# Performance work log

Measured on AMD Instinct MI355X. Metric: run time of the kernel, lower is better.

Reference implementation:

```python
import jax, jax.numpy as jnp
import numpy as np

N_EMBD = 1024
N_HEAD = 16

def _lin_params(key, fan_in, fan_out):
    kw, kb = jax.random.split(key)
    bound = 1.0 / np.sqrt(fan_in)
    W = jax.random.uniform(kw, (fan_in, fan_out), minval=-bound, maxval=bound, dtype=jnp.float32)
    b = jax.random.uniform(kb, (fan_out,), minval=-bound, maxval=bound, dtype=jnp.float32)
    return W, b

def setup_inputs() -> dict:
    key = jax.random.key(0)
    ks = jax.random.split(key, 6)
    x = jax.random.normal(ks[0], (2, 2048, N_EMBD), dtype=jnp.float32)
    W_attn, b_attn = _lin_params(ks[1], N_EMBD, 3 * N_EMBD)
    W_proj, b_proj = _lin_params(ks[2], N_EMBD, N_EMBD)
    W_fc, b_fc = _lin_params(ks[3], N_EMBD, 4 * N_EMBD)
    W_fc2, b_fc2 = _lin_params(ks[4], 4 * N_EMBD, N_EMBD)
    ln1_g = jnp.ones((N_EMBD,), jnp.float32); ln1_b = jnp.zeros((N_EMBD,), jnp.float32)
    ln2_g = jnp.ones((N_EMBD,), jnp.float32); ln2_b = jnp.zeros((N_EMBD,), jnp.float32)
    return {"x": x, "W_attn": W_attn, "b_attn": b_attn, "W_proj": W_proj, "b_proj": b_proj,
            "W_fc": W_fc, "b_fc": b_fc, "W_fc2": W_fc2, "b_fc2": b_fc2,
            "ln1_g": ln1_g, "ln1_b": ln1_b, "ln2_g": ln2_g, "ln2_b": ln2_b}

def _layernorm(x, g, b, eps=1e-5):
    mu = jnp.mean(x, axis=-1, keepdims=True)
    var = jnp.var(x, axis=-1, keepdims=True)
    return (x - mu) * jax.lax.rsqrt(var + eps) * g + b

def _attention(x, W_attn, b_attn, W_proj, b_proj):
    B, T, C = x.shape
    hd = C // N_HEAD
    qkv = x @ W_attn + b_attn                      # [B,T,3C]
    q, k, v = jnp.split(qkv, 3, axis=-1)
    # [B,T,C] -> [B,H,T,hd]
    q = q.reshape(B, T, N_HEAD, hd).transpose(0, 2, 1, 3)
    k = k.reshape(B, T, N_HEAD, hd).transpose(0, 2, 1, 3)
    v = v.reshape(B, T, N_HEAD, hd).transpose(0, 2, 1, 3)
    att = jnp.einsum('bhqd,bhkd->bhqk', q, k) * (1.0 / np.sqrt(hd))
    causal = jnp.tril(jnp.ones((T, T), bool))
    att = jnp.where(causal[None, None], att, -jnp.inf)
    att = jax.nn.softmax(att, axis=-1)
    y = jnp.einsum('bhqk,bhkd->bhqd', att, v)      # [B,H,T,hd]
    y = y.transpose(0, 2, 1, 3).reshape(B, T, C)
    return y @ W_proj + b_proj

def _mlp(x, W_fc, b_fc, W_fc2, b_fc2):
    h = jax.nn.gelu(x @ W_fc + b_fc, approximate=False)
    return h @ W_fc2 + b_fc2

def reference(x, W_attn, b_attn, W_proj, b_proj, W_fc, b_fc, W_fc2, b_fc2,
              ln1_g, ln1_b, ln2_g, ln2_b):
    x = x + _attention(_layernorm(x, ln1_g, ln1_b), W_attn, b_attn, W_proj, b_proj)
    x = x + _mlp(_layernorm(x, ln2_g, ln2_b), W_fc, b_fc, W_fc2, b_fc2)
    return x
```

## Files before the change

kernel.cpp:

```cpp
#include <hip/hip_runtime.h>
#include <cstdint>
#include <cstddef>


typedef unsigned short u16;
typedef short bf16x8 __attribute__((ext_vector_type(8)));
typedef float f32x4 __attribute__((ext_vector_type(4)));

#define C_EMBD 1024
#define T_SEQ  2048
#define N_BATCH 2
#define N_HEADS 16
#define HEAD_D 64
#define M_TOK  4096
#define Q_SCALE 0.18033688011112042f

__device__ __forceinline__ u16 f2b(float f) {
  union { float f; unsigned u; } v; v.f = f;
  unsigned r = (v.u + 0x7fffu + ((v.u >> 16) & 1u)) >> 16;
  return (u16)r;
}
__device__ __forceinline__ float b2f(u16 u) {
  union { unsigned u; float f; } v; v.u = ((unsigned)u) << 16;
  return v.f;
}
__device__ __forceinline__ unsigned pk2(float a, float b) {
  union { float f; unsigned u; } x, y; x.f = a; y.f = b;
  return __builtin_amdgcn_perm(y.u, x.u, 0x07060302u);
}
__device__ __forceinline__ void load_lds16(const void* g, void* l) {
  __builtin_amdgcn_global_load_lds(
      (const __attribute__((address_space(1))) void*)g,
      (__attribute__((address_space(3))) void*)l, 16, 0, 0);
}
__device__ __forceinline__ float gelu_fast(float x) {
  const float p = x * __builtin_fmaf(0.044715f * x, x, 1.0f);
  const float t = __builtin_amdgcn_exp2f(2.3021859215f * p);
  return x * t * __builtin_amdgcn_rcpf(t + 1.0f);
}

__global__ __launch_bounds__(256) void transpose_cast_all(
    const float* __restrict__ W0, u16* __restrict__ D0,
    const float* __restrict__ W1, u16* __restrict__ D1,
    const float* __restrict__ W2, u16* __restrict__ D2,
    const float* __restrict__ W3, u16* __restrict__ D3) {
  int id = blockIdx.x;
  const float* W; u16* D; int K, N, t;
  if (id < 3072)      { W = W0; D = D0; K = 1024; N = 3072; t = id; }
  else if (id < 4096) { W = W1; D = D1; K = 1024; N = 1024; t = id - 3072; }
  else if (id < 8192) { W = W2; D = D2; K = 1024; N = 4096; t = id - 4096; }
  else                { W = W3; D = D3; K = 4096; N = 1024; t = id - 8192; }
  const int nTN = N >> 5;
  const int n0 = (t % nTN) * 32, k0 = (t / nTN) * 32;
  __shared__ float tile[32][33];
  const int tx = threadIdx.x & 31, ty = threadIdx.x >> 5;
#pragma unroll
  for (int i = 0; i < 32; i += 8)
    tile[ty + i][tx] = W[(size_t)(k0 + ty + i) * N + n0 + tx];
  __syncthreads();
#pragma unroll
  for (int i = 0; i < 32; i += 8)
    D[(size_t)(n0 + ty + i) * K + k0 + tx] = f2b(tile[tx][ty + i]);
}

__global__ __launch_bounds__(256) void ln_cast(
    const float* __restrict__ X, const float* __restrict__ g,
    const float* __restrict__ b, u16* __restrict__ Y) {
  const int row = blockIdx.x;
  const int tid = threadIdx.x;
  const float4 v = ((const float4*)(X + (size_t)row * C_EMBD))[tid];
  float s = v.x + v.y + v.z + v.w;
  float ss = v.x * v.x + v.y * v.y + v.z * v.z + v.w * v.w;
#pragma unroll
  for (int off = 32; off > 0; off >>= 1) {
    s += __shfl_down(s, off, 64);
    ss += __shfl_down(ss, off, 64);
  }
  __shared__ float red[8];
  __shared__ float stats[2];
  const int wave = tid >> 6, lane = tid & 63;
  if (lane == 0) { red[wave] = s; red[4 + wave] = ss; }
  __syncthreads();
  if (tid == 0) {
    float S = red[0] + red[1] + red[2] + red[3];
    float SS = red[4] + red[5] + red[6] + red[7];
    float mu = S * (1.0f / C_EMBD);
    float var = SS * (1.0f / C_EMBD) - mu * mu;
    stats[0] = mu;
    stats[1] = rsqrtf(var + 1e-5f);
  }
  __syncthreads();
  const float mu = stats[0], rs = stats[1];
  const float4 gv = ((const float4*)g)[tid];
  const float4 bv = ((const float4*)b)[tid];
  ushort4 o;
  o.x = f2b((v.x - mu) * rs * gv.x + bv.x);
  o.y = f2b((v.y - mu) * rs * gv.y + bv.y);
  o.z = f2b((v.z - mu) * rs * gv.z + bv.z);
  o.w = f2b((v.w - mu) * rs * gv.w + bv.w);
  ((ushort4*)(Y + (size_t)row * C_EMBD))[tid] = o;
}

__global__ __launch_bounds__(256) void ln_reduce_cast(
    const float* __restrict__ P0, const float* __restrict__ P1,
    const float* __restrict__ bias, const float* __restrict__ res,
    const float* __restrict__ g, const float* __restrict__ b,
    float* __restrict__ X1, u16* __restrict__ Y) {
  const int row = blockIdx.x;
  const int tid = threadIdx.x;
  const size_t base = (size_t)row * C_EMBD;
  const float4 p0 = ((const float4*)(P0 + base))[tid];
  const float4 p1 = ((const float4*)(P1 + base))[tid];
  const float4 rr = ((const float4*)(res + base))[tid];
  const float4 bb = ((const float4*)bias)[tid];
  float4 v;
  v.x = p0.x + p1.x + rr.x + bb.x;
  v.y = p0.y + p1.y + rr.y + bb.y;
  v.z = p0.z + p1.z + rr.z + bb.z;
  v.w = p0.w + p1.w + rr.w + bb.w;
  ((float4*)(X1 + base))[tid] = v;
  float s = v.x + v.y + v.z + v.w;
  float ss = v.x * v.x + v.y * v.y + v.z * v.z + v.w * v.w;
#pragma unroll
  for (int off = 32; off > 0; off >>= 1) {
    s += __shfl_down(s, off, 64);
    ss += __shfl_down(ss, off, 64);
  }
  __shared__ float red[8];
  __shared__ float stats[2];
  const int wave = tid >> 6, lane = tid & 63;
  if (lane == 0) { red[wave] = s; red[4 + wave] = ss; }
  __syncthreads();
  if (tid == 0) {
    float S = red[0] + red[1] + red[2] + red[3];
    float SS = red[4] + red[5] + red[6] + red[7];
    float mu = S * (1.0f / C_EMBD);
    float var = SS * (1.0f / C_EMBD) - mu * mu;
    stats[0] = mu;
    stats[1] = rsqrtf(var + 1e-5f);
  }
  __syncthreads();
  const float mu = stats[0], rs = stats[1];
  const float4 gv = ((const float4*)g)[tid];
  const float4 bv = ((const float4*)b)[tid];
  ushort4 o;
  o.x = f2b((v.x - mu) * rs * gv.x + bv.x);
  o.y = f2b((v.y - mu) * rs * gv.y + bv.y);
  o.z = f2b((v.z - mu) * rs * gv.z + bv.z);
  o.w = f2b((v.w - mu) * rs * gv.w + bv.w);
  ((ushort4*)(Y + base))[tid] = o;
}

enum { EPI_BF16 = 0, EPI_GELU_BF16 = 2, EPI_PART = 3, EPI_QKV = 4 };

template <int EPI, int SPLIT>
__global__ __launch_bounds__(256) void gemm_bt(
    const u16* __restrict__ A, const u16* __restrict__ Bt,
    const float* __restrict__ bias,
    void* __restrict__ Cout, void* __restrict__ Cout2, void* __restrict__ Cout3,
    int M, int N, int K) {
  __shared__ u16 As[128 * 64];
  __shared__ u16 Bs[128 * 64];
  const int tid = threadIdx.x;
  const int wave = tid >> 6, lane = tid & 63;
  const int quad = lane >> 4, l16 = lane & 15;
  const int sw = l16 & 7;

  const int id = (int)blockIdx.y * (int)gridDim.x + (int)blockIdx.x;
  const int mt = ((id & 7) << 2) + ((id >> 3) & 3);
  const int nt_ = id >> 5;
  const int m0 = mt * 128, n0 = nt_ * 128;

  const int wm = (wave >> 1) * 64, wn = (wave & 1) * 64;

  f32x4 acc[4][4] = {};

  size_t aOff[4], bOff[4];
  int ldsOff[4];
#pragma unroll
  for (int i = 0; i < 4; ++i) {
    const int c = tid + i * 256;
    const int row = c >> 3, gc = ((c & 7) ^ (row & 7)) * 8;
    aOff[i] = (size_t)(m0 + row) * K + gc;
    bOff[i] = (size_t)(n0 + row) * K + gc;
    ldsOff[i] = c * 8;
  }

  const int kTiles = (K >> 6) / SPLIT;
  const int kt0 = (SPLIT == 2) ? (int)blockIdx.z * kTiles : 0;
  for (int kt = kt0; kt < kt0 + kTiles; ++kt) {
    const int k0 = kt << 6;
#pragma unroll
    for (int i = 0; i < 4; ++i)
      load_lds16(A + aOff[i] + k0, &As[ldsOff[i]]);
#pragma unroll
    for (int i = 0; i < 4; ++i)
      load_lds16(Bt + bOff[i] + k0, &Bs[ldsOff[i]]);
    __syncthreads();
#pragma unroll
    for (int ks = 0; ks < 2; ++ks) {
      bf16x8 aF[4], bF[4];
#pragma unroll
      for (int t = 0; t < 4; ++t) {
        aF[t] = *(const bf16x8*)
            &As[(wm + t * 16 + l16) * 64 + (((ks * 4 + quad) ^ sw) * 8)];
        bF[t] = *(const bf16x8*)
            &Bs[(wn + t * 16 + l16) * 64 + (((ks * 4 + quad) ^ sw) * 8)];
      }
#pragma unroll
      for (int tm = 0; tm < 4; ++tm)
#pragma unroll
        for (int tn = 0; tn < 4; ++tn)
          acc[tm][tn] = __builtin_amdgcn_mfma_f32_16x16x32_bf16(
              bF[tn], aF[tm], acc[tm][tn], 0, 0, 0);
    }
    __syncthreads();
  }

  float* Pz = (float*)((SPLIT == 2 && blockIdx.z == 1) ? Cout2 : Cout);
#pragma unroll
  for (int tm = 0; tm < 4; ++tm) {
    const int row = m0 + wm + tm * 16 + l16;
#pragma unroll
    for (int tn = 0; tn < 4; ++tn) {
      const int col = n0 + wn + tn * 16 + quad * 4;
      if constexpr (EPI == EPI_PART) {
        *(float4*)&Pz[(size_t)row * N + col] = *(float4*)&acc[tm][tn];
      } else {
        const float4 bz = *(const float4*)&bias[col];
        float v0 = acc[tm][tn][0] + bz.x, v1 = acc[tm][tn][1] + bz.y;
        float v2 = acc[tm][tn][2] + bz.z, v3 = acc[tm][tn][3] + bz.w;
        if constexpr (EPI == EPI_GELU_BF16) {
          v0 = gelu_fast(v0); v1 = gelu_fast(v1);
          v2 = gelu_fast(v2); v3 = gelu_fast(v3);
        }
        ushort4 o;
        o.x = f2b(v0); o.y = f2b(v1); o.z = f2b(v2); o.w = f2b(v3);
        *(ushort4*)&((u16*)Cout)[(size_t)row * N + col] = o;
      }
    }
  }
}

#define PHASE(MQ, NQ, STG, POST)                                              \
  {                                                                           \
    bf16x8 aF[4][2], bF[2][2];                                                \
    const u16* Ab_ = &lds[(size_t)((((MQ)*2 + par)) << 13)];                  \
    const u16* Bb_ = &lds[(size_t)(((2 + (NQ)) * 2 + par) << 13)];            \
    _Pragma("unroll") for (int t_ = 0; t_ < 4; ++t_)                          \
      _Pragma("unroll") for (int ks = 0; ks < 2; ++ks)                        \
        aF[t_][ks] = *(const bf16x8*)&Ab_[(wm * 64 + t_ * 16 + l16) * 64 +    \
                                          (((ks * 4 + quad) ^ sw) << 3)];     \
    _Pragma("unroll") for (int u_ = 0; u_ < 2; ++u_)                          \
      _Pragma("unroll") for (int ks = 0; ks < 2; ++ks)                        \
        bF[u_][ks] = *(const bf16x8*)&Bb_[(wn * 32 + u_ * 16 + l16) * 64 +    \
                                          (((ks * 4 + quad) ^ sw) << 3)];     \
    STG;                                                                      \
    __builtin_amdgcn_s_barrier();                                             \
    asm volatile("s_waitcnt lgkmcnt(0)" ::: "memory");                        \
    __builtin_amdgcn_s_setprio(1);                                            \
    _Pragma("unroll") for (int t_ = 0; t_ < 4; ++t_)                          \
      _Pragma("unroll") for (int u_ = 0; u_ < 2; ++u_)                        \
        _Pragma("unroll") for (int ks = 0; ks < 2; ++ks)                      \
          acc[(MQ)*4 + t_][(NQ)*2 + u_] =                                     \
              __builtin_amdgcn_mfma_f32_16x16x32_bf16(                        \
                  bF[u_][ks], aF[t_][ks], acc[(MQ)*4 + t_][(NQ)*2 + u_],      \
                  0, 0, 0);                                                   \
    __builtin_amdgcn_s_setprio(0);                                            \
    POST;                                                                     \
    __builtin_amdgcn_s_barrier();                                             \
  }

template <int EPI, int SPLIT>
__global__ __launch_bounds__(512, 2) void gemm256(
    const u16* __restrict__ A, const u16* __restrict__ Bt,
    const float* __restrict__ bias,
    void* __restrict__ Cout, void* __restrict__ Cout2,
    void* __restrict__ Cout3, void* __restrict__ Cout4,
    int M, int N, int K) {
  __shared__ u16 lds[8 * 8192];
  const int tid = threadIdx.x;
  const int lane = tid & 63;
  const int wave = tid >> 6;
  const int quad = lane >> 4, l16 = lane & 15;
  const int sw = l16 & 7;
  const int wm = wave >> 2, wn = wave & 3;

  const int nwg = (int)gridDim.x;
  const int rawid = (int)blockIdx.x;
  const int id = (rawid & 7) * (nwg >> 3) + (rawid >> 3);
  const int nTM = M >> 8;
  const int mt = id % nTM, ntl = id / nTM;
  const int m0 = mt << 8, n0 = ntl << 8;

  f32x4 acc[8][4] = {};

  size_t aOffs[2][2], bOffs[2][2];
  int ldsc[2];
#pragma unroll
  for (int i = 0; i < 2; ++i) {
    const int c = tid + i * 512;
    const int r = c >> 3;
    const int scc = ((c & 7) ^ (r & 7)) << 3;
    ldsc[i] = c * 8;
    const int ra = ((r >> 6) << 7) + (r & 63);
    const int rb = ((r >> 5) << 6) + (r & 31);
    aOffs[0][i] = (size_t)(m0 + ra) * K + scc;
    aOffs[1][i] = (size_t)(m0 + ra + 64) * K + scc;
    bOffs[0][i] = (size_t)(n0 + rb) * K + scc;
    bOffs[1][i] = (size_t)(n0 + rb + 32) * K + scc;
  }
  auto stA = [&](int mq, int p, int kt) {
    u16* dst = &lds[(size_t)((mq * 2 + p) << 13)];
    const int k0 = kt << 6;
#pragma unroll
    for (int i = 0; i < 2; ++i)
      load_lds16(A + aOffs[mq][i] + k0, dst + ldsc[i]);
  };
  auto stB = [&](int nq, int p, int kt) {
    u16* dst = &lds[(size_t)(((2 + nq) * 2 + p) << 13)];
    const int k0 = kt << 6;
#pragma unroll
    for (int i = 0; i < 2; ++i)
      load_lds16(Bt + bOffs[nq][i] + k0, dst + ldsc[i]);
  };

  const int NT = (K >> 6) / SPLIT;
  const int kt0 = (SPLIT > 1) ? (int)blockIdx.z * NT : 0;

  stA(0, 0, kt0); stB(0, 0, kt0); stA(1, 0, kt0); stB(1, 0, kt0);
  stB(0, 1, kt0 + 1); stA(0, 1, kt0 + 1);
  asm volatile("s_waitcnt vmcnt(4)" ::: "memory");
  __builtin_amdgcn_s_barrier();

  for (int t = 0; t < NT; t += 2) {
    {
      const int par = 0;
      const int k1 = kt0 + (t + 1 < NT ? t + 1 : 0);
      const int k2 = kt0 + (t + 2 < NT ? t + 2 : 0);
      PHASE(0, 0, stA(1, 1, k1), );
      PHASE(1, 0, stB(1, 1, k1), );
      PHASE(0, 1, stB(0, 0, k2), );
      PHASE(1, 1, stA(0, 0, k2),
            asm volatile("s_waitcnt vmcnt(4)" ::: "memory"));
    }
    {
      const int par = 1;
      const int k1 = kt0 + (t + 2 < NT ? t + 2 : 0);
      const int k2 = kt0 + (t + 3 < NT ? t + 3 : 0);
      PHASE(0, 0, stA(1, 0, k1), );
      PHASE(1, 0, stB(1, 0, k1), );
      PHASE(0, 1, stB(0, 1, k2), );
      PHASE(1, 1, stA(0, 1, k2),
            asm volatile("s_waitcnt vmcnt(4)" ::: "memory"));
    }
  }
  asm volatile("s_waitcnt vmcnt(0)" ::: "memory");

  if constexpr (EPI == EPI_PART) {
    const int z = (SPLIT > 1) ? (int)blockIdx.z : 0;
    float* Pz = (float*)(z == 0 ? Cout : z == 1 ? Cout2
                                       : z == 2 ? Cout3 : Cout4);
#pragma unroll
    for (int tm = 0; tm < 8; ++tm) {
      const int row = m0 + wm * 128 + tm * 16 + l16;
#pragma unroll
      for (int tn = 0; tn < 4; ++tn) {
        const int col = n0 + wn * 64 + tn * 16 + quad * 4;
        *(float4*)&Pz[(size_t)row * N + col] = *(float4*)&acc[tm][tn];
      }
    }
  } else if constexpr (EPI == EPI_QKV) {
#pragma unroll
    for (int tm = 0; tm < 8; ++tm) {
      const int row = m0 + wm * 128 + tm * 16 + l16;
      const int bb = row >> 11, tt = row & (T_SEQ - 1);
#pragma unroll
      for (int tn = 0; tn < 4; ++tn) {
        const int col = n0 + wn * 64 + tn * 16 + quad * 4;
        const float4 bz = *(const float4*)&bias[col];
        float v0 = acc[tm][tn][0] + bz.x, v1 = acc[tm][tn][1] + bz.y;
        float v2 = acc[tm][tn][2] + bz.z, v3 = acc[tm][tn][3] + bz.w;
        const int sec = col >> 10;
        const int h = (col & 1023) >> 6, d4 = col & 63;
        const int bh = bb * N_HEADS + h;
        if (sec == 0) {
          ushort4 o;
          o.x = f2b(v0 * Q_SCALE); o.y = f2b(v1 * Q_SCALE);
          o.z = f2b(v2 * Q_SCALE); o.w = f2b(v3 * Q_SCALE);
          *(ushort4*)&((u16*)Cout)[((size_t)bh * T_SEQ + tt) * HEAD_D + d4] = o;
        } else if (sec == 1) {
          ushort4 o;
          o.x = f2b(v0); o.y = f2b(v1); o.z = f2b(v2); o.w = f2b(v3);
          *(ushort4*)&((u16*)Cout2)[((size_t)bh * T_SEQ + tt) * HEAD_D + d4] = o;
        } else {
          u16* vp = (u16*)Cout3 + ((size_t)bh * HEAD_D + d4) * T_SEQ + tt;
          vp[0] = f2b(v0); vp[T_SEQ] = f2b(v1);
          vp[2 * T_SEQ] = f2b(v2); vp[3 * T_SEQ] = f2b(v3);
        }
      }
    }
  } else {
#pragma unroll
    for (int tm = 0; tm < 8; ++tm) {
      const int row = m0 + wm * 128 + tm * 16 + l16;
#pragma unroll
      for (int tn = 0; tn < 4; ++tn) {
        const int col = n0 + wn * 64 + tn * 16 + quad * 4;
        const float4 bz = *(const float4*)&bias[col];
        float v0 = acc[tm][tn][0] + bz.x, v1 = acc[tm][tn][1] + bz.y;
        float v2 = acc[tm][tn][2] + bz.z, v3 = acc[tm][tn][3] + bz.w;
        if constexpr (EPI == EPI_GELU_BF16) {
          v0 = gelu_fast(v0); v1 = gelu_fast(v1);
          v2 = gelu_fast(v2); v3 = gelu_fast(v3);
        }
        ushort4 o;
        o.x = f2b(v0); o.y = f2b(v1); o.z = f2b(v2); o.w = f2b(v3);
        *(ushort4*)&((u16*)Cout)[(size_t)row * N + col] = o;
      }
    }
  }
}

__global__ __launch_bounds__(256) void reduce_add4(
    const float* __restrict__ P0, const float* __restrict__ P1,
    const float* __restrict__ P2, const float* __restrict__ P3,
    const float* __restrict__ bias, const float* __restrict__ res,
    float* __restrict__ out) {
  const int idx = blockIdx.x * 256 + threadIdx.x;
  const float4 a = ((const float4*)P0)[idx];
  const float4 b = ((const float4*)P1)[idx];
  const float4 c = ((const float4*)P2)[idx];
  const float4 d = ((const float4*)P3)[idx];
  const float4 r = ((const float4*)res)[idx];
  const float4 g = ((const float4*)bias)[idx & 255];
  float4 o;
  o.x = a.x + b.x + c.x + d.x + r.x + g.x;
  o.y = a.y + b.y + c.y + d.y + r.y + g.y;
  o.z = a.z + b.z + c.z + d.z + r.z + g.z;
  o.w = a.w + b.w + c.w + d.w + r.w + g.w;
  ((float4*)out)[idx] = o;
}

__global__ __launch_bounds__(256) void attn_fwd(
    const u16* __restrict__ Q, const u16* __restrict__ Kb,
    const u16* __restrict__ Vt, u16* __restrict__ Y) {
  const int id = (int)blockIdx.y * (int)gridDim.x + (int)blockIdx.x;
  const int bh = (id & 7) + (((id >> 3) & 3) << 3);
  const int pair = id >> 5;
  const int nqt = (int)(T_SEQ / 64);
  const int tid = threadIdx.x;
  const int wave = tid >> 6, lane = tid & 63;
  const int quad = lane >> 4, l16 = lane & 15;
  const int sw = l16 & 7;
  const u16* Qp = Q + (size_t)bh * T_SEQ * HEAD_D;
  const u16* Kp = Kb + (size_t)bh * T_SEQ * HEAD_D;
  const u16* Vp = Vt + (size_t)bh * HEAD_D * T_SEQ;

  __shared__ u16 Ks[2][64 * 64];
  __shared__ u16 Vs[2][64 * 64];
  __shared__ u16 Pl[4][16 * 72];

  const int c1 = tid, c2 = tid + 256;
  const int r1 = c1 >> 3, g1 = ((c1 & 7) ^ (r1 & 7)) * 8;
  const int r2 = c2 >> 3, g2 = ((c2 & 7) ^ (r2 & 7)) * 8;
  const size_t kO1 = (size_t)r1 * HEAD_D + g1, kO2 = (size_t)r2 * HEAD_D + g2;
  const size_t vO1 = (size_t)r1 * T_SEQ + g1, vO2 = (size_t)r2 * T_SEQ + g2;
  u16* const dK1[2] = {&Ks[0][c1 * 8], &Ks[1][c1 * 8]};
  u16* const dK2[2] = {&Ks[0][c2 * 8], &Ks[1][c2 * 8]};
  u16* const dV1[2] = {&Vs[0][c1 * 8], &Vs[1][c1 * 8]};
  u16* const dV2[2] = {&Vs[0][c2 * 8], &Vs[1][c2 * 8]};

  auto stageK = [&](int bb, int k0) {
    const u16* base = Kp + (size_t)k0 * HEAD_D;
    load_lds16(base + kO1, dK1[bb]);
    load_lds16(base + kO2, dK2[bb]);
  };
  auto stageV = [&](int bb, int k0) {
    const u16* base = Vp + k0;
    load_lds16(base + vO1, dV1[bb]);
    load_lds16(base + vO2, dV2[bb]);
  };

  const int b = bh >> 4, h = bh & 15;

#pragma unroll 1
  for (int phase = 0; phase < 2; ++phase) {
    const int qb = phase == 0 ? (nqt - 1 - pair) : pair;
    const int q0 = qb * 64;
    const int qglob = q0 + wave * 16 + l16;

    if (phase == 1) __syncthreads();

    bf16x8 qF[2];
    qF[0] = *(const bf16x8*)&Qp[(size_t)qglob * HEAD_D + quad * 8];
    qF[1] = *(const bf16x8*)&Qp[(size_t)qglob * HEAD_D + 32 + quad * 8];

    f32x4 o[4] = {};
    float mrun = -3e38f, lrun = 0.0f;

    stageK(0, 0);
    stageV(0, 0);

    int buf = 0;
    for (int kb = 0; kb <= qb; ++kb) {
      const int k0 = kb * 64;
      __syncthreads();
      if (kb < qb) {
        stageK(buf ^ 1, k0 + 64);
        stageV(buf ^ 1, k0 + 64);
      }
      f32x4 st[4] = {};
#pragma unroll
      for (int ks = 0; ks < 2; ++ks) {
#pragma unroll
        for (int nt = 0; nt < 4; ++nt) {
          bf16x8 kF = *(const bf16x8*)
              &Ks[buf][(nt * 16 + l16) * 64 + (((ks * 4 + quad) ^ sw) * 8)];
          st[nt] = __builtin_amdgcn_mfma_f32_16x16x32_bf16(kF, qF[ks], st[nt],
                                                           0, 0, 0);
        }
      }
      if (kb == qb) {
#pragma unroll
        for (int nt = 0; nt < 4; ++nt) {
#pragma unroll
          for (int r = 0; r < 4; ++r) {
            const int key = k0 + nt * 16 + quad * 4 + r;
            if (key > qglob) st[nt][r] = -3e38f;
          }
        }
      }
      float m = st[0][0];
#pragma unroll
      for (int nt = 0; nt < 4; ++nt)
#pragma unroll
        for (int r = 0; r < 4; ++r) m = fmaxf(m, st[nt][r]);
      m = fmaxf(m, __shfl_xor(m, 16, 64));
      m = fmaxf(m, __shfl_xor(m, 32, 64));
      const float nm = fmaxf(mrun, m);
      const float alpha = __builtin_amdgcn_exp2f(mrun - nm);
      mrun = nm;
      float sum = 0.0f;
#pragma unroll
      for (int nt = 0; nt < 4; ++nt)
#pragma unroll
        for (int r = 0; r < 4; ++r) {
          const float p = __builtin_amdgcn_exp2f(st[nt][r] - nm);
          st[nt][r] = p;
          sum += p;
        }
      sum += __shfl_xor(sum, 16, 64);
      sum += __shfl_xor(sum, 32, 64);
      lrun = lrun * alpha + sum;
#pragma unroll
      for (int nt = 0; nt < 4; ++nt)
#pragma unroll
        for (int r = 0; r < 4; ++r) o[nt][r] *= alpha;
#pragma unroll
      for (int nt = 0; nt < 4; ++nt) {
        uint2 pk;
        pk.x = pk2(st[nt][0], st[nt][1]);
        pk.y = pk2(st[nt][2], st[nt][3]);
        *(uint2*)&Pl[wave][l16 * 72 + nt * 16 + quad * 4] = pk;
      }
#pragma unroll
      for (int ks = 0; ks < 2; ++ks) {
        bf16x8 aP = *(const bf16x8*)&Pl[wave][l16 * 72 + ks * 32 + quad * 8];
#pragma unroll
        for (int nt = 0; nt < 4; ++nt) {
          bf16x8 vF = *(const bf16x8*)
              &Vs[buf][(nt * 16 + l16) * 64 + (((ks * 4 + quad) ^ sw) * 8)];
          o[nt] =
              __builtin_amdgcn_mfma_f32_16x16x32_bf16(vF, aP, o[nt], 0, 0, 0);
        }
      }
      buf ^= 1;
    }

    const float rl = 1.0f / lrun;
    u16* yp = Y + ((size_t)(b * T_SEQ + qglob)) * C_EMBD + h * HEAD_D;
#pragma unroll
    for (int nt = 0; nt < 4; ++nt) {
      ushort4 ov;
      ov.x = f2b(o[nt][0] * rl); ov.y = f2b(o[nt][1] * rl);
      ov.z = f2b(o[nt][2] * rl); ov.w = f2b(o[nt][3] * rl);
      *(ushort4*)&yp[nt * 16 + quad * 4] = ov;
    }
  }
}

extern "C" void kernel_launch(void* const* d_in, const int* in_sizes, int n_in,
                              void* d_out, int out_size, void* d_ws,
                              size_t ws_size, hipStream_t stream) {
  const float* x      = (const float*)d_in[0];
  const float* W_attn = (const float*)d_in[1];
  const float* b_attn = (const float*)d_in[2];
  const float* W_proj = (const float*)d_in[3];
  const float* b_proj = (const float*)d_in[4];
  const float* W_fc   = (const float*)d_in[5];
  const float* b_fc   = (const float*)d_in[6];
  const float* W_fc2  = (const float*)d_in[7];
  const float* b_fc2  = (const float*)d_in[8];
  const float* ln1_g  = (const float*)d_in[9];
  const float* ln1_b  = (const float*)d_in[10];
  const float* ln2_g  = (const float*)d_in[11];
  const float* ln2_b  = (const float*)d_in[12];

  u16* wfc2T = (u16*)d_ws;
  float* x1  = (float*)(wfc2T + (size_t)1024 * 4096);
  u16* hbuf  = (u16*)(x1 + (size_t)M_TOK * C_EMBD);
  u16* dead  = hbuf + (size_t)M_TOK * 4096;
  u16* wqkvT = dead;
  u16* wprojT = wqkvT + (size_t)3072 * 1024;
  u16* wfcT  = wprojT + (size_t)1024 * 1024;
  u16* Abuf  = wfcT + (size_t)4096 * 1024;
  u16* Qb    = Abuf + (size_t)M_TOK * C_EMBD;
  u16* Kbuf  = Qb + (size_t)32 * T_SEQ * HEAD_D;
  u16* Vtb   = Kbuf + (size_t)32 * T_SEQ * HEAD_D;

  float* projP = (float*)hbuf;
  float* fc2P1 = (float*)dead;
  float* fc2P2 = fc2P1 + (size_t)M_TOK * C_EMBD;
  float* fc2P3 = fc2P2 + (size_t)M_TOK * C_EMBD;

  const dim3 blk(256);
  const dim3 blk512(512);

  transpose_cast_all<<<12288, blk, 0, stream>>>(
      W_attn, wqkvT, W_proj, wprojT, W_fc, wfcT, W_fc2, wfc2T);

  ln_cast<<<M_TOK, blk, 0, stream>>>(x, ln1_g, ln1_b, Abuf);

  gemm256<EPI_QKV, 1><<<dim3(192), blk512, 0, stream>>>(
      Abuf, wqkvT, b_attn, Qb, Kbuf, Vtb, nullptr, M_TOK, 3072, 1024);

  attn_fwd<<<dim3(T_SEQ / 128, 32), blk, 0, stream>>>(Qb, Kbuf, Vtb, Abuf);

  gemm_bt<EPI_PART, 2><<<dim3(1024 / 128, M_TOK / 128, 2), blk, 0, stream>>>(
      Abuf, wprojT, nullptr, projP, projP + (size_t)M_TOK * C_EMBD, nullptr,
      M_TOK, 1024, 1024);
  ln_reduce_cast<<<M_TOK, blk, 0, stream>>>(
      projP, projP + (size_t)M_TOK * C_EMBD, b_proj, x, ln2_g, ln2_b,
      x1, Abuf);

  gemm256<EPI_GELU_BF16, 1><<<dim3(256), blk512, 0, stream>>>(
      Abuf, wfcT, b_fc, hbuf, nullptr, nullptr, nullptr, M_TOK, 4096, 1024);

  gemm256<EPI_PART, 4><<<dim3(64, 1, 4), blk512, 0, stream>>>(
      hbuf, wfc2T, nullptr, d_out, fc2P1, fc2P2, fc2P3, M_TOK, 1024, 4096);
  reduce_add4<<<M_TOK * C_EMBD / 1024, blk, 0, stream>>>(
      (const float*)d_out, fc2P1, fc2P2, fc2P3, b_fc2, x1, (float*)d_out);
}
```

Measured before the change: 343.5 us.

## Reschedule GEMM phases for fragment reuse and restructure attention grid and softmax

The GEMM main loop is reordered so the A fragments and two B fragment sets are reused across phases, which cuts repeated LDS fragment loads and drops one lgkmcnt wait. The attention kernel now gives each block a single query tile, launched heaviest-first over a 1D grid with an XCD-aware mapping and a launch-bounds occupancy hint, instead of pairing two tiles per block. It also skips the online-softmax rescale unless the running max grows by more than a threshold, and swizzles the P scratch buffer in place of padding it. These changes trade more blocks and extra register pressure for less per-block imbalance and less ALU and LDS work, and the lazy rescale relies on exp2 values staying within range.

```diff
diff --git a/kernel.cpp b/kernel.cpp
--- a/kernel.cpp
+++ b/kernel.cpp
@@ -242,34 +242,29 @@
   }
 }
 
-#define PHASE(MQ, NQ, STG, POST)                                              \
-  {                                                                           \
-    bf16x8 aF[4][2], bF[2][2];                                                \
-    const u16* Ab_ = &lds[(size_t)((((MQ)*2 + par)) << 13)];                  \
-    const u16* Bb_ = &lds[(size_t)(((2 + (NQ)) * 2 + par) << 13)];            \
+#define G_LOADA(MQ, PAR)                                                      \
+  { const u16* Ab_ = &lds[(unsigned)((((MQ)*2 + (PAR))) << 13)];              \
     _Pragma("unroll") for (int t_ = 0; t_ < 4; ++t_)                          \
       _Pragma("unroll") for (int ks = 0; ks < 2; ++ks)                        \
         aF[t_][ks] = *(const bf16x8*)&Ab_[(wm * 64 + t_ * 16 + l16) * 64 +    \
-                                          (((ks * 4 + quad) ^ sw) << 3)];     \
+                                          (((ks * 4 + quad) ^ sw) << 3)]; }
+#define G_LOADB(BV, NQ, PAR)                                                  \
+  { const u16* Bb_ = &lds[(unsigned)(((2 + (NQ)) * 2 + (PAR)) << 13)];        \
     _Pragma("unroll") for (int u_ = 0; u_ < 2; ++u_)                          \
       _Pragma("unroll") for (int ks = 0; ks < 2; ++ks)                        \
-        bF[u_][ks] = *(const bf16x8*)&Bb_[(wn * 32 + u_ * 16 + l16) * 64 +    \
-                                          (((ks * 4 + quad) ^ sw) << 3)];     \
-    STG;                                                                      \
-    __builtin_amdgcn_s_barrier();                                             \
-    asm volatile("s_waitcnt lgkmcnt(0)" ::: "memory");                        \
-    __builtin_amdgcn_s_setprio(1);                                            \
+        BV[u_][ks] = *(const bf16x8*)&Bb_[(wn * 32 + u_ * 16 + l16) * 64 +    \
+                                          (((ks * 4 + quad) ^ sw) << 3)]; }
+#define G_MMA(MQ, NQ, BV)                                                     \
     _Pragma("unroll") for (int t_ = 0; t_ < 4; ++t_)                          \
       _Pragma("unroll") for (int u_ = 0; u_ < 2; ++u_)                        \
         _Pragma("unroll") for (int ks = 0; ks < 2; ++ks)                      \
           acc[(MQ)*4 + t_][(NQ)*2 + u_] =                                     \
               __builtin_amdgcn_mfma_f32_16x16x32_bf16(                        \
-                  bF[u_][ks], aF[t_][ks], acc[(MQ)*4 + t_][(NQ)*2 + u_],      \
-                  0, 0, 0);                                                   \
-    __builtin_amdgcn_s_setprio(0);                                            \
-    POST;                                                                     \
-    __builtin_amdgcn_s_barrier();                                             \
-  }
+                  BV[u_][ks], aF[t_][ks], acc[(MQ)*4 + t_][(NQ)*2 + u_],      \
+                  0, 0, 0);
+#define G_BAR()   __builtin_amdgcn_s_barrier()
+#define G_LGKM0() asm volatile("s_waitcnt lgkmcnt(0)" ::: "memory")
+#define G_PRIO(x) __builtin_amdgcn_s_setprio(x)
 
 template <int EPI, int SPLIT>
 __global__ __launch_bounds__(512, 2) void gemm256(
@@ -331,28 +326,30 @@
   stA(0, 0, kt0); stB(0, 0, kt0); stA(1, 0, kt0); stB(1, 0, kt0);
   stB(0, 1, kt0 + 1); stA(0, 1, kt0 + 1);
   asm volatile("s_waitcnt vmcnt(4)" ::: "memory");
-  __builtin_amdgcn_s_barrier();
+  G_BAR();
+
+  bf16x8 aF[4][2];
+  bf16x8 bF0[2][2], bF1[2][2];
 
   for (int t = 0; t < NT; t += 2) {
-    {
-      const int par = 0;
-      const int k1 = kt0 + (t + 1 < NT ? t + 1 : 0);
-      const int k2 = kt0 + (t + 2 < NT ? t + 2 : 0);
-      PHASE(0, 0, stA(1, 1, k1), );
-      PHASE(1, 0, stB(1, 1, k1), );
-      PHASE(0, 1, stB(0, 0, k2), );
-      PHASE(1, 1, stA(0, 0, k2),
-            asm volatile("s_waitcnt vmcnt(4)" ::: "memory"));
-    }
-    {
-      const int par = 1;
-      const int k1 = kt0 + (t + 2 < NT ? t + 2 : 0);
-      const int k2 = kt0 + (t + 3 < NT ? t + 3 : 0);
-      PHASE(0, 0, stA(1, 0, k1), );
-      PHASE(1, 0, stB(1, 0, k1), );
-      PHASE(0, 1, stB(0, 1, k2), );
-      PHASE(1, 1, stA(0, 1, k2),
-            asm volatile("s_waitcnt vmcnt(4)" ::: "memory"));
+#pragma unroll
+    for (int p = 0; p < 2; ++p) {
+      const int par = p;
+      const int k1 = kt0 + (t + 1 + p < NT ? t + 1 + p : 0);
+      const int k2 = kt0 + (t + 2 + p < NT ? t + 2 + p : 0);
+      G_LOADA(0, par); G_LOADB(bF0, 0, par);
+      stA(1, par ^ 1, k1);
+      G_BAR(); G_LGKM0(); G_PRIO(1); G_MMA(0, 0, bF0); G_PRIO(0); G_BAR();
+      G_LOADB(bF1, 1, par);
+      stB(1, par ^ 1, k1);
+      G_BAR(); G_LGKM0(); G_PRIO(1); G_MMA(0, 1, bF1); G_PRIO(0); G_BAR();
+      G_LOADA(1, par);
+      stA(0, par, k2);
+      G_BAR(); G_LGKM0(); G_PRIO(1); G_MMA(1, 0, bF0); G_PRIO(0); G_BAR();
+      stB(0, par, k2);
+      G_BAR(); G_PRIO(1); G_MMA(1, 1, bF1); G_PRIO(0);
+      asm volatile("s_waitcnt vmcnt(4)" ::: "memory");
+      G_BAR();
     }
   }
   asm volatile("s_waitcnt vmcnt(0)" ::: "memory");
@@ -442,13 +439,13 @@
   ((float4*)out)[idx] = o;
 }
 
-__global__ __launch_bounds__(256) void attn_fwd(
+__global__ __launch_bounds__(256, 4) void attn_fwd(
     const u16* __restrict__ Q, const u16* __restrict__ Kb,
     const u16* __restrict__ Vt, u16* __restrict__ Y) {
-  const int id = (int)blockIdx.y * (int)gridDim.x + (int)blockIdx.x;
-  const int bh = (id & 7) + (((id >> 3) & 3) << 3);
-  const int pair = id >> 5;
-  const int nqt = (int)(T_SEQ / 64);
+  const int id = (int)blockIdx.x;
+  const int xcd = id & 7, slot = id >> 3;
+  const int bh = xcd + ((slot & 3) << 3);
+  const int qb = (T_SEQ / 64 - 1) - (slot >> 2);
   const int tid = threadIdx.x;
   const int wave = tid >> 6, lane = tid & 63;
   const int quad = lane >> 4, l16 = lane & 15;
@@ -459,7 +456,7 @@
 
   __shared__ u16 Ks[2][64 * 64];
   __shared__ u16 Vs[2][64 * 64];
-  __shared__ u16 Pl[4][16 * 72];
+  __shared__ u16 Pl[4][16 * 64];
 
   const int c1 = tid, c2 = tid + 256;
   const int r1 = c1 >> 3, g1 = ((c1 & 7) ^ (r1 & 7)) * 8;
@@ -483,110 +480,108 @@
   };
 
   const int b = bh >> 4, h = bh & 15;
-
-#pragma unroll 1
-  for (int phase = 0; phase < 2; ++phase) {
-    const int qb = phase == 0 ? (nqt - 1 - pair) : pair;
-    const int q0 = qb * 64;
-    const int qglob = q0 + wave * 16 + l16;
-
-    if (phase == 1) __syncthreads();
-
-    bf16x8 qF[2];
-    qF[0] = *(const bf16x8*)&Qp[(size_t)qglob * HEAD_D + quad * 8];
-    qF[1] = *(const bf16x8*)&Qp[(size_t)qglob * HEAD_D + 32 + quad * 8];
-
-    f32x4 o[4] = {};
-    float mrun = -3e38f, lrun = 0.0f;
-
-    stageK(0, 0);
-    stageV(0, 0);
-
-    int buf = 0;
-    for (int kb = 0; kb <= qb; ++kb) {
-      const int k0 = kb * 64;
-      __syncthreads();
-      if (kb < qb) {
-        stageK(buf ^ 1, k0 + 64);
-        stageV(buf ^ 1, k0 + 64);
-      }
-      f32x4 st[4] = {};
-#pragma unroll
-      for (int ks = 0; ks < 2; ++ks) {
-#pragma unroll
-        for (int nt = 0; nt < 4; ++nt) {
-          bf16x8 kF = *(const bf16x8*)
-              &Ks[buf][(nt * 16 + l16) * 64 + (((ks * 4 + quad) ^ sw) * 8)];
-          st[nt] = __builtin_amdgcn_mfma_f32_16x16x32_bf16(kF, qF[ks], st[nt],
-                                                           0, 0, 0);
+  const int q0 = qb * 64;
+  const int qglob = q0 + wave * 16 + l16;
+
+  bf16x8 qF[2];
+  qF[0] = *(const bf16x8*)&Qp[(size_t)qglob * HEAD_D + quad * 8];
+  qF[1] = *(const bf16x8*)&Qp[(size_t)qglob * HEAD_D + 32 + quad * 8];
+
+  f32x4 o[4] = {};
+  float mrun = -3e38f, lrun = 0.0f;
+
+  stageK(0, 0);
+  stageV(0, 0);
+
+  int buf = 0;
+  for (int kb = 0; kb <= qb; ++kb) {
+    const int k0 = kb * 64;
+    __syncthreads();
+    if (kb < qb) {
+      stageK(buf ^ 1, k0 + 64);
+      stageV(buf ^ 1, k0 + 64);
+    }
+    f32x4 st[4] = {};
+#pragma unroll
+    for (int ks = 0; ks < 2; ++ks) {
+#pragma unroll
+      for (int nt = 0; nt < 4; ++nt) {
+        bf16x8 kF = *(const bf16x8*)
+            &Ks[buf][(nt * 16 + l16) * 64 + (((ks * 4 + quad) ^ sw) * 8)];
+        st[nt] = __builtin_amdgcn_mfma_f32_16x16x32_bf16(kF, qF[ks], st[nt],
+                                                         0, 0, 0);
+      }
+    }
+    if (kb == qb) {
+#pragma unroll
+      for (int nt = 0; nt < 4; ++nt) {
+#pragma unroll
+        for (int r = 0; r < 4; ++r) {
+          const int key = k0 + nt * 16 + quad * 4 + r;
+          if (key > qglob) st[nt][r] = -3e38f;
         }
       }
-      if (kb == qb) {
-#pragma unroll
-        for (int nt = 0; nt < 4; ++nt) {
-#pragma unroll
-          for (int r = 0; r < 4; ++r) {
-            const int key = k0 + nt * 16 + quad * 4 + r;
-            if (key > qglob) st[nt][r] = -3e38f;
-          }
-        }
-      }
-      float m = st[0][0];
-#pragma unroll
-      for (int nt = 0; nt < 4; ++nt)
-#pragma unroll
-        for (int r = 0; r < 4; ++r) m = fmaxf(m, st[nt][r]);
-      m = fmaxf(m, __shfl_xor(m, 16, 64));
-      m = fmaxf(m, __shfl_xor(m, 32, 64));
+    }
+    float m = st[0][0];
+#pragma unroll
+    for (int nt = 0; nt < 4; ++nt)
+#pragma unroll
+      for (int r = 0; r < 4; ++r) m = fmaxf(m, st[nt][r]);
+    m = fmaxf(m, __shfl_xor(m, 16, 64));
+    m = fmaxf(m, __shfl_xor(m, 32, 64));
+    if (!__all(m - mrun <= 8.0f)) {
       const float nm = fmaxf(mrun, m);
       const float alpha = __builtin_amdgcn_exp2f(mrun - nm);
       mrun = nm;
-      float sum = 0.0f;
+      lrun *= alpha;
 #pragma unroll
       for (int nt = 0; nt < 4; ++nt)
 #pragma unroll
-        for (int r = 0; r < 4; ++r) {
-          const float p = __builtin_amdgcn_exp2f(st[nt][r] - nm);
-          st[nt][r] = p;
-          sum += p;
-        }
-      sum += __shfl_xor(sum, 16, 64);
-      sum += __shfl_xor(sum, 32, 64);
-      lrun = lrun * alpha + sum;
-#pragma unroll
-      for (int nt = 0; nt < 4; ++nt)
-#pragma unroll
         for (int r = 0; r < 4; ++r) o[nt][r] *= alpha;
+    }
+    float sum = 0.0f;
+#pragma unroll
+    for (int nt = 0; nt < 4; ++nt)
+#pragma unroll
+      for (int r = 0; r < 4; ++r) {
+        const float p = __builtin_amdgcn_exp2f(st[nt][r] - mrun);
+        st[nt][r] = p;
+        sum += p;
+      }
+    sum += __shfl_xor(sum, 16, 64);
+    sum += __shfl_xor(sum, 32, 64);
+    lrun += sum;
+#pragma unroll
+    for (int nt = 0; nt < 4; ++nt) {
+      uint2 pk;
+      pk.x = pk2(st[nt][0], st[nt][1]);
+      pk.y = pk2(st[nt][2], st[nt][3]);
+      const int wc = (((2 * nt + (quad >> 1)) ^ sw) << 3) + ((quad & 1) << 2);
+      *(uint2*)&Pl[wave][(l16 << 6) + wc] = pk;
+    }
+#pragma unroll
+    for (int ks = 0; ks < 2; ++ks) {
+      bf16x8 aP = *(const bf16x8*)
+          &Pl[wave][(l16 << 6) + (((ks * 4 + quad) ^ sw) << 3)];
 #pragma unroll
       for (int nt = 0; nt < 4; ++nt) {
-        uint2 pk;
-        pk.x = pk2(st[nt][0], st[nt][1]);
-        pk.y = pk2(st[nt][2], st[nt][3]);
-        *(uint2*)&Pl[wave][l16 * 72 + nt * 16 + quad * 4] = pk;
-      }
-#pragma unroll
-      for (int ks = 0; ks < 2; ++ks) {
-        bf16x8 aP = *(const bf16x8*)&Pl[wave][l16 * 72 + ks * 32 + quad * 8];
-#pragma unroll
-        for (int nt = 0; nt < 4; ++nt) {
-          bf16x8 vF = *(const bf16x8*)
-              &Vs[buf][(nt * 16 + l16) * 64 + (((ks * 4 + quad) ^ sw) * 8)];
-          o[nt] =
-              __builtin_amdgcn_mfma_f32_16x16x32_bf16(vF, aP, o[nt], 0, 0, 0);
-        }
-      }
-      buf ^= 1;
-    }
-
-    const float rl = 1.0f / lrun;
-    u16* yp = Y + ((size_t)(b * T_SEQ + qglob)) * C_EMBD + h * HEAD_D;
-#pragma unroll
-    for (int nt = 0; nt < 4; ++nt) {
-      ushort4 ov;
-      ov.x = f2b(o[nt][0] * rl); ov.y = f2b(o[nt][1] * rl);
-      ov.z = f2b(o[nt][2] * rl); ov.w = f2b(o[nt][3] * rl);
-      *(ushort4*)&yp[nt * 16 + quad * 4] = ov;
-    }
+        bf16x8 vF = *(const bf16x8*)
+            &Vs[buf][(nt * 16 + l16) * 64 + (((ks * 4 + quad) ^ sw) * 8)];
+        o[nt] =
+            __builtin_amdgcn_mfma_f32_16x16x32_bf16(vF, aP, o[nt], 0, 0, 0);
+      }
+    }
+    buf ^= 1;
+  }
+
+  const float rl = 1.0f / lrun;
+  u16* yp = Y + ((size_t)(b * T_SEQ + qglob)) * C_EMBD + h * HEAD_D;
+#pragma unroll
+  for (int nt = 0; nt < 4; ++nt) {
+    ushort4 ov;
+    ov.x = f2b(o[nt][0] * rl); ov.y = f2b(o[nt][1] * rl);
+    ov.z = f2b(o[nt][2] * rl); ov.w = f2b(o[nt][3] * rl);
+    *(ushort4*)&yp[nt * 16 + quad * 4] = ov;
   }
 }
 
@@ -635,7 +630,7 @@
   gemm256<EPI_QKV, 1><<<dim3(192), blk512, 0, stream>>>(
       Abuf, wqkvT, b_attn, Qb, Kbuf, Vtb, nullptr, M_TOK, 3072, 1024);
 
-  attn_fwd<<<dim3(T_SEQ / 128, 32), blk, 0, stream>>>(Qb, Kbuf, Vtb, Abuf);
+  attn_fwd<<<dim3(1024), blk, 0, stream>>>(Qb, Kbuf, Vtb, Abuf);
 
   gemm_bt<EPI_PART, 2><<<dim3(1024 / 128, M_TOK / 128, 2), blk, 0, stream>>>(
       Abuf, wprojT, nullptr, projP, projP + (size_t)M_TOK * C_EMBD, nullptr,
```

New measurement: 324.0 us. 5.7% less time.
